# Optimization experiments

Measured on AMD Instinct MI355X. Metric: run time of the kernel, lower is better.

The kernel has to match this reference:

```python
import jax, jax.numpy as jnp
import numpy as np

B_J0 = 0.01   # baseline threshold
DT = 1.0
BETA = 1.8    # adaptation strength
LENS = 0.5
SCALE = 6.0
HIGHT = 0.15
GAMMA = 0.5


def _gauss(x, mu, sigma):
    return jnp.exp(-(x - mu) ** 2 / (2.0 * sigma ** 2)) / jnp.sqrt(2.0 * jnp.pi) / sigma


@jax.custom_vjp
def spike_fn(x):
    return (x > 0).astype(x.dtype)


def _spike_fwd(x):
    return spike_fn(x), x


def _spike_bwd(x, g):
    # multi-gaussian surrogate gradient (config.gradient_type == 'MG')
    temp = (_gauss(x, 0.0, LENS) * (1.0 + HIGHT)
            - _gauss(x, LENS, SCALE * LENS) * HIGHT
            - _gauss(x, -LENS, SCALE * LENS) * HIGHT)
    return (g * temp * GAMMA,)


spike_fn.defvjp(_spike_fwd, _spike_bwd)


def setup_inputs() -> dict:
    key = jax.random.key(0)
    ks = jax.random.split(key, 20)
    Bt, T, I, H, O = 256, 250, 700, 128, 20
    f32 = jnp.float32
    return {
        'x': jax.random.uniform(ks[0], (Bt, T, I), dtype=f32),
        'mask': jnp.ones((2, H, H), dtype=f32),
        'w_ih1': (jax.random.normal(ks[1], (I, H), dtype=f32) / np.sqrt(I).astype(np.float32)),
        'b_ih1': jnp.zeros((H,), f32),
        'w_h1h1': (jax.random.normal(ks[2], (H, H), dtype=f32) / np.sqrt(H).astype(np.float32)),
        'b_h1h1': jnp.zeros((H,), f32),
        'w_h1h2': (jax.random.normal(ks[3], (H, H), dtype=f32) / np.sqrt(H).astype(np.float32)),
        'b_h1h2': jnp.zeros((H,), f32),
        'w_h2h2': (jax.random.normal(ks[4], (H, H), dtype=f32) / np.sqrt(H).astype(np.float32)),
        'b_h2h2': jnp.zeros((H,), f32),
        'w_h2o': (jax.random.normal(ks[5], (H, O), dtype=f32) / np.sqrt(H).astype(np.float32)),
        'b_h2o': jnp.zeros((O,), f32),
        'tau_adp_h1': 150.0 + 10.0 * jax.random.normal(ks[6], (H,), dtype=f32),
        'tau_adp_h2': 150.0 + 10.0 * jax.random.normal(ks[7], (H,), dtype=f32),
        'tau_m_h1': 20.0 + 5.0 * jax.random.normal(ks[8], (H,), dtype=f32),
        'tau_m_h2': 20.0 + 5.0 * jax.random.normal(ks[9], (H,), dtype=f32),
        'tau_m_o': 20.0 + 5.0 * jax.random.normal(ks[10], (O,), dtype=f32),
        'hid1_mem0': jax.random.uniform(ks[11], (Bt, H), dtype=f32),
        'hid2_mem0': jax.random.uniform(ks[12], (Bt, H), dtype=f32),
        'out_mem0': jax.random.uniform(ks[13], (Bt, O), dtype=f32),
    }


def _forward(x, mask, w_ih1, b_ih1, w_h1h1, b_h1h1, w_h1h2, b_h1h2,
             w_h2h2, b_h2h2, w_h2o, b_h2o, tau_adp_h1, tau_adp_h2,
             tau_m_h1, tau_m_h2, tau_m_o, hid1_mem0, hid2_mem0, out_mem0):
    Bt, T, _ = x.shape
    H = w_ih1.shape[1]
    O = w_h2o.shape[1]
    # dropout mask applied to recurrent weights (weights stored [in, out])
    w11 = w_h1h1 * mask[0]
    w22 = w_h2h2 * mask[1]
    a1 = jnp.exp(-DT / tau_m_h1)
    r1 = jnp.exp(-DT / tau_adp_h1)
    a2 = jnp.exp(-DT / tau_m_h2)
    r2 = jnp.exp(-DT / tau_adp_h2)
    ao = jnp.exp(-DT / tau_m_o)
    # precompute input projection for all timesteps: [T, B, H]
    xin = jnp.einsum('bti,ih->tbh', x, w_ih1) + b_ih1

    def step(carry, inps):
        h1m, h1s, h2m, h2s, om, b1, b2, acc, s1, s2 = carry
        xt, t = inps
        # layer 1 (adaptive LIF)
        i1 = xt + h1s @ w11 + b_h1h1
        b1 = r1 * b1 + (1.0 - r1) * h1s
        B1 = B_J0 + BETA * b1
        h1m = h1m * a1 + (1.0 - a1) * i1 - B1 * h1s * DT
        h1s = spike_fn(h1m - B1)
        s1 = s1 + h1s
        # layer 2 (adaptive LIF)
        i2 = h1s @ w_h1h2 + b_h1h2 + h2s @ w22 + b_h2h2
        b2 = r2 * b2 + (1.0 - r2) * h2s
        B2 = B_J0 + BETA * b2
        h2m = h2m * a2 + (1.0 - a2) * i2 - B2 * h2s * DT
        h2s = spike_fn(h2m - B2)
        s2 = s2 + h2s
        # leaky-integrator readout (no spike)
        io = h2s @ w_h2o + b_h2o
        om = om * ao + (1.0 - ao) * io
        acc = acc + jnp.where(t > 10, jax.nn.softmax(om, axis=-1), 0.0)
        return (h1m, h1s, h2m, h2s, om, b1, b2, acc, s1, s2), None

    zH = jnp.zeros((Bt, H), x.dtype)
    carry0 = (hid1_mem0, zH, hid2_mem0, zH, out_mem0,
              jnp.full((Bt, H), B_J0, x.dtype), jnp.full((Bt, H), B_J0, x.dtype),
              jnp.zeros((Bt, O), x.dtype), zH, zH)
    carry, _ = jax.lax.scan(step, carry0, (xin, jnp.arange(T)))
    output, s1, s2 = carry[7], carry[8], carry[9]
    A_norm = jnp.sum(jnp.abs(w11)) + jnp.sum(jnp.abs(w22))
    return output, s1 / T, s2 / T, A_norm


def reference(x, mask, w_ih1, b_ih1, w_h1h1, b_h1h1, w_h1h2, b_h1h2,
              w_h2h2, b_h2h2, w_h2o, b_h2o, tau_adp_h1, tau_adp_h2,
              tau_m_h1, tau_m_h2, tau_m_o, hid1_mem0, hid2_mem0, out_mem0):
    return _forward(x, mask, w_ih1, b_ih1, w_h1h1, b_h1h1, w_h1h2, b_h1h2,
                    w_h2h2, b_h2h2, w_h2o, b_h2o, tau_adp_h1, tau_adp_h2,
                    tau_m_h1, tau_m_h2, tau_m_o, hid1_mem0, hid2_mem0, out_mem0)
```

## Files before the change

### kernel.cpp

```cpp
#include <hip/hip_runtime.h>
#include <math.h>

#define TT 250
#define BT 256
#define HN 128
#define ON 20
#define KIN 700
#define NKT 22

#define XIN_OFF 0
#define WPKH_OFF 8192000
#define WPKL_OFF 8237056

typedef __attribute__((ext_vector_type(8))) short bf16x8;
typedef __attribute__((ext_vector_type(4))) float f32x4;

__device__ __forceinline__ unsigned short bf16rne(float f) {
    unsigned u = __float_as_uint(f);
    unsigned r = u + 0x7fffu + ((u >> 16) & 1u);
    return (unsigned short)(r >> 16);
}
__device__ __forceinline__ void hilo(float v, short& h, short& l) {
    unsigned short hh = bf16rne(v);
    float vh = __uint_as_float((unsigned)hh << 16);
    h = (short)hh;
    l = (short)bf16rne(v - vh);
}

__global__ __launch_bounds__(256) void packw(const float* __restrict__ w,
                                             unsigned short* __restrict__ ph,
                                             unsigned short* __restrict__ pl) {
    int i = blockIdx.x * 256 + threadIdx.x;
    int k = i >> 7, c = i & 127;
    float v = (k < KIN) ? w[k * HN + c] : 0.f;
    short h, l;
    hilo(v, h, l);
    int dst = (((k >> 5) * 8 + (c >> 4)) * 64 + (((k >> 3) & 3) * 16 + (c & 15))) * 8 + (k & 7);
    ph[dst] = (unsigned short)h;
    pl[dst] = (unsigned short)l;
}

__global__ __launch_bounds__(256) void gemm_in(const float* __restrict__ x,
        const bf16x8* __restrict__ wph, const bf16x8* __restrict__ wpl,
        const float* __restrict__ bias1, const float* __restrict__ bias2,
        float* __restrict__ xin) {
    const int tid = threadIdx.x;
    const int w = tid >> 6, lane = tid & 63;
    const int q = lane >> 4, li = lane & 15;
    const long mrow = (long)blockIdx.x * 64 + w * 16 + li;
    const float* xr = x + mrow * KIN + q * 8;

    float b12[8];
#pragma unroll
    for (int nt = 0; nt < 8; nt++) {
        int col = nt * 16 + li;
        b12[nt] = bias1[col] + bias2[col];
    }

    f32x4 acc[8];
#pragma unroll
    for (int nt = 0; nt < 8; nt++) acc[nt] = (f32x4){0.f, 0.f, 0.f, 0.f};

    for (int kt = 0; kt < NKT; kt++) {
        float av[8];
        const float* p = xr + kt * 32;
        *(float4*)&av[0] = *(const float4*)p;
        if (kt == NKT - 1 && q == 3) {
            av[4] = 0.f; av[5] = 0.f; av[6] = 0.f; av[7] = 0.f;
        } else {
            *(float4*)&av[4] = *(const float4*)(p + 4);
        }
        bf16x8 ah, al;
#pragma unroll
        for (int j = 0; j < 8; j++) {
            short h, l;
            hilo(av[j], h, l);
            ah[j] = h; al[j] = l;
        }
#pragma unroll
        for (int nt = 0; nt < 8; nt++) {
            bf16x8 bh = wph[(kt * 8 + nt) * 64 + lane];
            bf16x8 bl = wpl[(kt * 8 + nt) * 64 + lane];
            acc[nt] = __builtin_amdgcn_mfma_f32_16x16x32_bf16(ah, bh, acc[nt], 0, 0, 0);
            acc[nt] = __builtin_amdgcn_mfma_f32_16x16x32_bf16(al, bh, acc[nt], 0, 0, 0);
            acc[nt] = __builtin_amdgcn_mfma_f32_16x16x32_bf16(ah, bl, acc[nt], 0, 0, 0);
        }
    }

#pragma unroll
    for (int r = 0; r < 4; r++) {
        int m = blockIdx.x * 64 + w * 16 + q * 4 + r;
        int bq = (int)(((unsigned long long)m * 67109ull) >> 24);
        int tt = m - bq * 250;
        float* dst = xin + ((size_t)tt * BT + bq) * HN;
#pragma unroll
        for (int nt = 0; nt < 8; nt++) dst[nt * 16 + li] = acc[nt][r] + b12[nt];
    }
}

__global__ __launch_bounds__(512, 2) void snn_scan(
    const float* __restrict__ xin, const float* __restrict__ mask,
    const float* __restrict__ w_h1h1, const float* __restrict__ w_h1h2,
    const float* __restrict__ b_h1h2, const float* __restrict__ w_h2h2,
    const float* __restrict__ b_h2h2, const float* __restrict__ w_h2o,
    const float* __restrict__ b_h2o, const float* __restrict__ tau_adp1,
    const float* __restrict__ tau_adp2, const float* __restrict__ taum1,
    const float* __restrict__ taum2, const float* __restrict__ taumo,
    const float* __restrict__ h1m0, const float* __restrict__ h2m0,
    const float* __restrict__ om0, float* __restrict__ out) {

    __shared__ __align__(16) unsigned short sA1[2 * 2048];
    __shared__ __align__(16) unsigned short sA2[2048];
    __shared__ float omb[16 * ON];
    __shared__ float red[8];

    const int tid = threadIdx.x;
    const int w = tid >> 6, lane = tid & 63;
    const int q = lane >> 4, li = lane & 15;
    const int col = w * 16 + li;
    const int r0 = blockIdx.x * 16;

    bf16x8 h11[4], l11[4], h22[4], l22[4], h12[4], l12[4], hO[4], lO[4];
    const int ocol = (w == 6) ? li : 16 + li;
    const bool oval = (w >= 6) && (ocol < ON);
    float pn = 0.f;
#pragma unroll
    for (int kt = 0; kt < 4; kt++) {
#pragma unroll
        for (int j = 0; j < 8; j++) {
            const int k = kt * 32 + q * 8 + j;
            const int idx = k * HN + col;
            float v11 = w_h1h1[idx] * mask[idx];
            float v22 = w_h2h2[idx] * mask[HN * HN + idx];
            float v12 = w_h1h2[idx];
            pn += fabsf(v11) + fabsf(v22);
            short hh, ll;
            hilo(v11, hh, ll); h11[kt][j] = hh; l11[kt][j] = ll;
            hilo(v22, hh, ll); h22[kt][j] = hh; l22[kt][j] = ll;
            hilo(v12, hh, ll); h12[kt][j] = hh; l12[kt][j] = ll;
            float vO = oval ? w_h2o[k * ON + ocol] : 0.f;
            hilo(vO, hh, ll); hO[kt][j] = hh; lO[kt][j] = ll;
        }
    }

    const float a1 = expf(-1.f / taum1[col]);
    const float r1 = expf(-1.f / tau_adp1[col]);
    const float a2 = expf(-1.f / taum2[col]);
    const float r2 = expf(-1.f / tau_adp2[col]);
    const float cc2 = b_h1h2[col] + b_h2h2[col];
    float h1m[4], h2m[4], b1[4], b2[4], c1[4], c2n[4];
    unsigned s1bits = 0, s2bits = 0;
#pragma unroll
    for (int r = 0; r < 4; r++) {
        h1m[r] = h1m0[(r0 + q * 4 + r) * HN + col];
        h2m[r] = h2m0[(r0 + q * 4 + r) * HN + col];
        b1[r] = 0.01f; b2[r] = 0.01f; c1[r] = 0.f; c2n[r] = 0.f;
    }
    const float ao = oval ? expf(-1.f / taumo[ocol]) : 0.f;
    const float bo = oval ? b_h2o[ocol] : 0.f;
    float om[4];
#pragma unroll
    for (int r = 0; r < 4; r++)
        om[r] = oval ? om0[(r0 + q * 4 + r) * ON + ocol] : 0.f;
    const int sm = lane >> 2, ob = (lane & 3) * 5;
    float accs[5] = {0.f, 0.f, 0.f, 0.f, 0.f};

    {
        unsigned* z1 = (unsigned*)sA1;
        unsigned* z2 = (unsigned*)sA2;
        z1[tid] = 0u; z1[tid + 512] = 0u;
        z2[tid] = 0u; z2[tid + 512] = 0u;
    }

#pragma unroll
    for (int off = 32; off > 0; off >>= 1) pn += __shfl_down(pn, off);
    if (lane == 0) red[w] = pn;
    __syncthreads();
    if (tid == 0 && blockIdx.x == 0) {
        float s = 0.f;
#pragma unroll
        for (int i = 0; i < 8; i++) s += red[i];
        out[70656] = s;
    }

    const int wbase = (w >> 1) * 512 + (((2 * w + (li >> 3)) & 3) * 16 + q * 4) * 8 + (li & 7);

    const bf16x8* sa1v = (const bf16x8*)sA1;
    const bf16x8* sa2v = (const bf16x8*)sA2;
    const unsigned short ONE = 0x3F80u;

    for (int t = 0; t < TT; t++) {
        const int rb = (t & 1) * 256;
        const int wb = ((t + 1) & 1) * 2048;

        float xt[4];
#pragma unroll
        for (int r = 0; r < 4; r++)
            xt[r] = xin[((size_t)t * BT + r0 + q * 4 + r) * HN + col];

        bf16x8 f1[4], f2[4];
#pragma unroll
        for (int kt = 0; kt < 4; kt++) {
            f1[kt] = sa1v[rb + kt * 64 + lane];
            f2[kt] = sa2v[kt * 64 + lane];
        }
        f32x4 aI = {0.f, 0.f, 0.f, 0.f}, aG = {0.f, 0.f, 0.f, 0.f};
#pragma unroll
        for (int kt = 0; kt < 4; kt++) {
            aI = __builtin_amdgcn_mfma_f32_16x16x32_bf16(f1[kt], h11[kt], aI, 0, 0, 0);
            aI = __builtin_amdgcn_mfma_f32_16x16x32_bf16(f1[kt], l11[kt], aI, 0, 0, 0);
            aG = __builtin_amdgcn_mfma_f32_16x16x32_bf16(f2[kt], h22[kt], aG, 0, 0, 0);
            aG = __builtin_amdgcn_mfma_f32_16x16x32_bf16(f2[kt], l22[kt], aG, 0, 0, 0);
        }
        if (w >= 6) {
            f32x4 aO = {0.f, 0.f, 0.f, 0.f};
#pragma unroll
            for (int kt = 0; kt < 4; kt++) {
                aO = __builtin_amdgcn_mfma_f32_16x16x32_bf16(f2[kt], hO[kt], aO, 0, 0, 0);
                aO = __builtin_amdgcn_mfma_f32_16x16x32_bf16(f2[kt], lO[kt], aO, 0, 0, 0);
            }
            if (t >= 1) {
#pragma unroll
                for (int r = 0; r < 4; r++) {
                    om[r] = ao * om[r] + (1.f - ao) * (bo + aO[r]);
                    if (oval) omb[(q * 4 + r) * ON + ocol] = om[r];
                }
            }
        }
#pragma unroll
        for (int r = 0; r < 4; r++) {
            const float sv = (float)((s1bits >> r) & 1u);
            const float i1 = xt[r] + aI[r];
            b1[r] = r1 * b1[r] + (1.f - r1) * sv;
            const float B = 0.01f + 1.8f * b1[r];
            h1m[r] = a1 * h1m[r] + (1.f - a1) * i1 - B * sv;
            const bool sp = (h1m[r] - B) > 0.f;
            s1bits = sp ? (s1bits | (1u << r)) : (s1bits & ~(1u << r));
            c1[r] += sp ? 1.f : 0.f;
            sA1[wb + wbase + r * 8] = sp ? ONE : (unsigned short)0;
        }
        __syncthreads();

        bf16x8 g1[4];
#pragma unroll
        for (int kt = 0; kt < 4; kt++) g1[kt] = sa1v[(wb >> 3) + kt * 64 + lane];
        f32x4 aJ = {0.f, 0.f, 0.f, 0.f};
#pragma unroll
        for (int kt = 0; kt < 4; kt++) {
            aJ = __builtin_amdgcn_mfma_f32_16x16x32_bf16(g1[kt], h12[kt], aJ, 0, 0, 0);
            aJ = __builtin_amdgcn_mfma_f32_16x16x32_bf16(g1[kt], l12[kt], aJ, 0, 0, 0);
        }
        if (w == 7 && t >= 12) {
            float v[5], e[5];
            float mx = -1e30f;
#pragma unroll
            for (int i = 0; i < 5; i++) { v[i] = omb[sm * ON + ob + i]; mx = fmaxf(mx, v[i]); }
            mx = fmaxf(mx, __shfl_xor(mx, 1));
            mx = fmaxf(mx, __shfl_xor(mx, 2));
            float se = 0.f;
#pragma unroll
            for (int i = 0; i < 5; i++) { e[i] = __expf(v[i] - mx); se += e[i]; }
            se += __shfl_xor(se, 1);
            se += __shfl_xor(se, 2);
            const float inv = 1.f / se;
#pragma unroll
            for (int i = 0; i < 5; i++) accs[i] += e[i] * inv;
        }
#pragma unroll
        for (int r = 0; r < 4; r++) {
            const float sv = (float)((s2bits >> r) & 1u);
            const float i2 = aJ[r] + aG[r] + cc2;
            b2[r] = r2 * b2[r] + (1.f - r2) * sv;
            const float B = 0.01f + 1.8f * b2[r];
            h2m[r] = a2 * h2m[r] + (1.f - a2) * i2 - B * sv;
            const bool sp = (h2m[r] - B) > 0.f;
            s2bits = sp ? (s2bits | (1u << r)) : (s2bits & ~(1u << r));
            c2n[r] += sp ? 1.f : 0.f;
            sA2[wbase + r * 8] = sp ? ONE : (unsigned short)0;
        }
        __syncthreads();
    }

    if (w >= 6) {
        bf16x8 f2[4];
#pragma unroll
        for (int kt = 0; kt < 4; kt++) f2[kt] = sa2v[kt * 64 + lane];
        f32x4 aO = {0.f, 0.f, 0.f, 0.f};
#pragma unroll
        for (int kt = 0; kt < 4; kt++) {
            aO = __builtin_amdgcn_mfma_f32_16x16x32_bf16(f2[kt], hO[kt], aO, 0, 0, 0);
            aO = __builtin_amdgcn_mfma_f32_16x16x32_bf16(f2[kt], lO[kt], aO, 0, 0, 0);
        }
#pragma unroll
        for (int r = 0; r < 4; r++) {
            om[r] = ao * om[r] + (1.f - ao) * (bo + aO[r]);
            if (oval) omb[(q * 4 + r) * ON + ocol] = om[r];
        }
    }
    __syncthreads();
    if (w == 7) {
        float v[5], e[5];
        float mx = -1e30f;
#pragma unroll
        for (int i = 0; i < 5; i++) { v[i] = omb[sm * ON + ob + i]; mx = fmaxf(mx, v[i]); }
        mx = fmaxf(mx, __shfl_xor(mx, 1));
        mx = fmaxf(mx, __shfl_xor(mx, 2));
        float se = 0.f;
#pragma unroll
        for (int i = 0; i < 5; i++) { e[i] = __expf(v[i] - mx); se += e[i]; }
        se += __shfl_xor(se, 1);
        se += __shfl_xor(se, 2);
        const float inv = 1.f / se;
#pragma unroll
        for (int i = 0; i < 5; i++) out[(r0 + sm) * ON + ob + i] = accs[i] + e[i] * inv;
    }
#pragma unroll
    for (int r = 0; r < 4; r++) {
        out[5120 + (r0 + q * 4 + r) * HN + col] = c1[r] * (1.f / 250.f);
        out[37888 + (r0 + q * 4 + r) * HN + col] = c2n[r] * (1.f / 250.f);
    }
}

extern "C" void kernel_launch(void* const* d_in, const int* in_sizes, int n_in,
                              void* d_out, int out_size, void* d_ws, size_t ws_size,
                              hipStream_t stream) {
    const float* x        = (const float*)d_in[0];
    const float* mask     = (const float*)d_in[1];
    const float* w_ih1    = (const float*)d_in[2];
    const float* b_ih1    = (const float*)d_in[3];
    const float* w_h1h1   = (const float*)d_in[4];
    const float* b_h1h1   = (const float*)d_in[5];
    const float* w_h1h2   = (const float*)d_in[6];
    const float* b_h1h2   = (const float*)d_in[7];
    const float* w_h2h2   = (const float*)d_in[8];
    const float* b_h2h2   = (const float*)d_in[9];
    const float* w_h2o    = (const float*)d_in[10];
    const float* b_h2o    = (const float*)d_in[11];
    const float* tau_adp1 = (const float*)d_in[12];
    const float* tau_adp2 = (const float*)d_in[13];
    const float* taum1    = (const float*)d_in[14];
    const float* taum2    = (const float*)d_in[15];
    const float* taumo    = (const float*)d_in[16];
    const float* h1m0     = (const float*)d_in[17];
    const float* h2m0     = (const float*)d_in[18];
    const float* om0      = (const float*)d_in[19];
    float* out = (float*)d_out;
    float* ws  = (float*)d_ws;

    float* xin = ws + XIN_OFF;
    unsigned short* wph = (unsigned short*)(ws + WPKH_OFF);
    unsigned short* wpl = (unsigned short*)(ws + WPKL_OFF);

    packw<<<352, 256, 0, stream>>>(w_ih1, wph, wpl);
    gemm_in<<<1000, 256, 0, stream>>>(x, (const bf16x8*)wph, (const bf16x8*)wpl,
                                      b_ih1, b_h1h1, xin);
    snn_scan<<<16, 512, 0, stream>>>(xin, mask, w_h1h1, w_h1h2, b_h1h2, w_h2h2,
                                     b_h2h2, w_h2o, b_h2o, tau_adp1, tau_adp2,
                                     taum1, taum2, taumo, h1m0, h2m0, om0, out);
}
```

Before: 655.8 us.

## Split scan hi/lo MFMA across 16 waves and stage GEMM weights in LDS

The recurrent scan kernel doubles its block to 1024 threads. Eight waves compute the high-bf16 weight products and run the neuron updates, while eight more waves compute the low-bf16 products and exchange partial sums through shared memory. Layer-2 work is skewed one step behind layer 1, so each timestep needs two barriers instead of a double-buffered spike array, and the readout softmax moves to a dedicated wave. The input GEMM now double-buffers the packed weight tiles in LDS instead of reading them from global memory per wave. The trade-offs are extra shared-memory traffic, larger blocks and more complex pipelining that could introduce off-by-one timing errors.

```diff
diff --git a/kernel.cpp b/kernel.cpp
--- a/kernel.cpp
+++ b/kernel.cpp
@@ -44,6 +44,7 @@
         const bf16x8* __restrict__ wph, const bf16x8* __restrict__ wpl,
         const float* __restrict__ bias1, const float* __restrict__ bias2,
         float* __restrict__ xin) {
+    __shared__ __align__(16) short Bs[2][2][4096];
     const int tid = threadIdx.x;
     const int w = tid >> 6, lane = tid & 63;
     const int q = lane >> 4, li = lane & 15;
@@ -52,39 +53,54 @@
 
     float b12[8];
 #pragma unroll
-    for (int nt = 0; nt < 8; nt++) {
-        int col = nt * 16 + li;
-        b12[nt] = bias1[col] + bias2[col];
-    }
+    for (int nt = 0; nt < 8; nt++) b12[nt] = bias1[nt * 16 + li] + bias2[nt * 16 + li];
 
     f32x4 acc[8];
 #pragma unroll
     for (int nt = 0; nt < 8; nt++) acc[nt] = (f32x4){0.f, 0.f, 0.f, 0.f};
 
+    {
+        bf16x8* dh = (bf16x8*)Bs[0][0];
+        bf16x8* dl = (bf16x8*)Bs[0][1];
+        dh[tid] = wph[tid]; dh[tid + 256] = wph[tid + 256];
+        dl[tid] = wpl[tid]; dl[tid + 256] = wpl[tid + 256];
+    }
+    __syncthreads();
+
     for (int kt = 0; kt < NKT; kt++) {
+        const int cur = kt & 1;
+        const bool more = (kt + 1 < NKT);
+        bf16x8 nh0, nh1, nl0, nl1;
+        if (more) {
+            const int base = (kt + 1) * 512 + tid;
+            nh0 = wph[base]; nh1 = wph[base + 256];
+            nl0 = wpl[base]; nl1 = wpl[base + 256];
+        }
         float av[8];
-        const float* p = xr + kt * 32;
-        *(float4*)&av[0] = *(const float4*)p;
-        if (kt == NKT - 1 && q == 3) {
-            av[4] = 0.f; av[5] = 0.f; av[6] = 0.f; av[7] = 0.f;
-        } else {
-            *(float4*)&av[4] = *(const float4*)(p + 4);
-        }
+        *(float4*)&av[0] = *(const float4*)(xr + kt * 32);
+        if (kt == NKT - 1 && q == 3) { av[4] = 0.f; av[5] = 0.f; av[6] = 0.f; av[7] = 0.f; }
+        else *(float4*)&av[4] = *(const float4*)(xr + kt * 32 + 4);
         bf16x8 ah, al;
 #pragma unroll
-        for (int j = 0; j < 8; j++) {
-            short h, l;
-            hilo(av[j], h, l);
-            ah[j] = h; al[j] = l;
-        }
+        for (int j = 0; j < 8; j++) { short h, l; hilo(av[j], h, l); ah[j] = h; al[j] = l; }
+
+        const bf16x8* bh = (const bf16x8*)Bs[cur][0];
+        const bf16x8* bl = (const bf16x8*)Bs[cur][1];
 #pragma unroll
         for (int nt = 0; nt < 8; nt++) {
-            bf16x8 bh = wph[(kt * 8 + nt) * 64 + lane];
-            bf16x8 bl = wpl[(kt * 8 + nt) * 64 + lane];
-            acc[nt] = __builtin_amdgcn_mfma_f32_16x16x32_bf16(ah, bh, acc[nt], 0, 0, 0);
-            acc[nt] = __builtin_amdgcn_mfma_f32_16x16x32_bf16(al, bh, acc[nt], 0, 0, 0);
-            acc[nt] = __builtin_amdgcn_mfma_f32_16x16x32_bf16(ah, bl, acc[nt], 0, 0, 0);
-        }
+            bf16x8 vh = bh[nt * 64 + lane];
+            bf16x8 vl = bl[nt * 64 + lane];
+            acc[nt] = __builtin_amdgcn_mfma_f32_16x16x32_bf16(ah, vh, acc[nt], 0, 0, 0);
+            acc[nt] = __builtin_amdgcn_mfma_f32_16x16x32_bf16(al, vh, acc[nt], 0, 0, 0);
+            acc[nt] = __builtin_amdgcn_mfma_f32_16x16x32_bf16(ah, vl, acc[nt], 0, 0, 0);
+        }
+        if (more) {
+            bf16x8* dh = (bf16x8*)Bs[cur ^ 1][0];
+            bf16x8* dl = (bf16x8*)Bs[cur ^ 1][1];
+            dh[tid] = nh0; dh[tid + 256] = nh1;
+            dl[tid] = nl0; dl[tid + 256] = nl1;
+        }
+        __syncthreads();
     }
 
 #pragma unroll
@@ -98,7 +114,9 @@
     }
 }
 
-__global__ __launch_bounds__(512, 2) void snn_scan(
+#define PST 20
+
+__global__ __launch_bounds__(1024) void snn_scan(
     const float* __restrict__ xin, const float* __restrict__ mask,
     const float* __restrict__ w_h1h1, const float* __restrict__ w_h1h2,
     const float* __restrict__ b_h1h2, const float* __restrict__ w_h2h2,
@@ -109,20 +127,28 @@
     const float* __restrict__ h1m0, const float* __restrict__ h2m0,
     const float* __restrict__ om0, float* __restrict__ out) {
 
-    __shared__ __align__(16) unsigned short sA1[2 * 2048];
-    __shared__ __align__(16) unsigned short sA2[2048];
-    __shared__ float omb[16 * ON];
-    __shared__ float red[8];
+    __shared__ __align__(16) unsigned short sF1[2048];
+    __shared__ __align__(16) unsigned short sF2[2048];
+    __shared__ __align__(16) float P11[HN * PST];
+    __shared__ __align__(16) float P12[HN * PST];
+    __shared__ __align__(16) float P22[HN * PST];
+    __shared__ __align__(16) float Ohi[ON * PST];
+    __shared__ __align__(16) float Olo[ON * PST];
+    __shared__ float red[16];
 
     const int tid = threadIdx.x;
     const int w = tid >> 6, lane = tid & 63;
     const int q = lane >> 4, li = lane & 15;
-    const int col = w * 16 + li;
+    const bool ishi = (w < 8);
+    const int g = w & 7;
+    const int col = g * 16 + li;
     const int r0 = blockIdx.x * 16;
 
-    bf16x8 h11[4], l11[4], h22[4], l22[4], h12[4], l12[4], hO[4], lO[4];
-    const int ocol = (w == 6) ? li : 16 + li;
-    const bool oval = (w >= 6) && (ocol < ON);
+    bf16x8 f11[4], f12[4], f22[4], fO[4];
+    const bool whoW = (w >= 12);
+    const int ocol = (w < 14) ? li : 16 + li;
+    const bool oval = whoW && (ocol < ON);
+    const bool oHi = (w == 12) || (w == 14);
     float pn = 0.f;
 #pragma unroll
     for (int kt = 0; kt < 4; kt++) {
@@ -133,44 +159,49 @@
             float v11 = w_h1h1[idx] * mask[idx];
             float v22 = w_h2h2[idx] * mask[HN * HN + idx];
             float v12 = w_h1h2[idx];
-            pn += fabsf(v11) + fabsf(v22);
-            short hh, ll;
-            hilo(v11, hh, ll); h11[kt][j] = hh; l11[kt][j] = ll;
-            hilo(v22, hh, ll); h22[kt][j] = hh; l22[kt][j] = ll;
-            hilo(v12, hh, ll); h12[kt][j] = hh; l12[kt][j] = ll;
+            if (ishi) pn += fabsf(v11) + fabsf(v22);
+            short h, l;
+            hilo(v11, h, l); f11[kt][j] = ishi ? h : l;
+            hilo(v22, h, l); f22[kt][j] = ishi ? h : l;
+            hilo(v12, h, l); f12[kt][j] = ishi ? h : l;
             float vO = oval ? w_h2o[k * ON + ocol] : 0.f;
-            hilo(vO, hh, ll); hO[kt][j] = hh; lO[kt][j] = ll;
-        }
-    }
-
-    const float a1 = expf(-1.f / taum1[col]);
-    const float r1 = expf(-1.f / tau_adp1[col]);
-    const float a2 = expf(-1.f / taum2[col]);
-    const float r2 = expf(-1.f / tau_adp2[col]);
-    const float cc2 = b_h1h2[col] + b_h2h2[col];
-    float h1m[4], h2m[4], b1[4], b2[4], c1[4], c2n[4];
+            hilo(vO, h, l); fO[kt][j] = oHi ? h : l;
+        }
+    }
+
+    float a1 = 0.f, r1c = 0.f, a2 = 0.f, r2c = 0.f, cc2 = 0.f;
+    float h1m[4], h2m[4], b1a[4], b2a[4], c1[4], c2n[4], xt[4];
     unsigned s1bits = 0, s2bits = 0;
-#pragma unroll
-    for (int r = 0; r < 4; r++) {
-        h1m[r] = h1m0[(r0 + q * 4 + r) * HN + col];
-        h2m[r] = h2m0[(r0 + q * 4 + r) * HN + col];
-        b1[r] = 0.01f; b2[r] = 0.01f; c1[r] = 0.f; c2n[r] = 0.f;
-    }
-    const float ao = oval ? expf(-1.f / taumo[ocol]) : 0.f;
-    const float bo = oval ? b_h2o[ocol] : 0.f;
-    float om[4];
-#pragma unroll
-    for (int r = 0; r < 4; r++)
-        om[r] = oval ? om0[(r0 + q * 4 + r) * ON + ocol] : 0.f;
+    if (ishi) {
+        a1 = expf(-1.f / taum1[col]);
+        r1c = expf(-1.f / tau_adp1[col]);
+        a2 = expf(-1.f / taum2[col]);
+        r2c = expf(-1.f / tau_adp2[col]);
+        cc2 = b_h1h2[col] + b_h2h2[col];
+#pragma unroll
+        for (int r = 0; r < 4; r++) {
+            h1m[r] = h1m0[(r0 + q * 4 + r) * HN + col];
+            h2m[r] = h2m0[(r0 + q * 4 + r) * HN + col];
+            b1a[r] = 0.01f; b2a[r] = 0.01f; c1[r] = 0.f; c2n[r] = 0.f;
+            xt[r] = xin[(size_t)(r0 + q * 4 + r) * HN + col];
+        }
+    }
     const int sm = lane >> 2, ob = (lane & 3) * 5;
-    float accs[5] = {0.f, 0.f, 0.f, 0.f, 0.f};
-
-    {
-        unsigned* z1 = (unsigned*)sA1;
-        unsigned* z2 = (unsigned*)sA2;
-        z1[tid] = 0u; z1[tid + 512] = 0u;
-        z2[tid] = 0u; z2[tid + 512] = 0u;
-    }
+    float om[5], accs[5], aoc[5], bjoc[5];
+    if (w == 15) {
+#pragma unroll
+        for (int i = 0; i < 5; i++) {
+            aoc[i] = expf(-1.f / taumo[ob + i]);
+            bjoc[i] = b_h2o[ob + i];
+            om[i] = om0[(r0 + sm) * ON + ob + i];
+            accs[i] = 0.f;
+        }
+    }
+
+    ((unsigned*)sF1)[tid] = 0u;
+    ((unsigned*)sF2)[tid] = 0u;
+    for (int i = tid; i < HN * PST; i += 1024) { P11[i] = 0.f; P12[i] = 0.f; P22[i] = 0.f; }
+    for (int i = tid; i < ON * PST; i += 1024) { Ohi[i] = 0.f; Olo[i] = 0.f; }
 
 #pragma unroll
     for (int off = 32; off > 0; off >>= 1) pn += __shfl_down(pn, off);
@@ -183,141 +214,194 @@
         out[70656] = s;
     }
 
-    const int wbase = (w >> 1) * 512 + (((2 * w + (li >> 3)) & 3) * 16 + q * 4) * 8 + (li & 7);
-
-    const bf16x8* sa1v = (const bf16x8*)sA1;
-    const bf16x8* sa2v = (const bf16x8*)sA2;
+    const int wbase = (w >> 1) * 512 + ((((2 * w + (li >> 3)) & 3) * 16 + q * 4) * 8) + (li & 7);
+    const int pidx = col * PST + q * 4;
+    const bf16x8* s1v = (const bf16x8*)sF1;
+    const bf16x8* s2v = (const bf16x8*)sF2;
     const unsigned short ONE = 0x3F80u;
 
+    f32x4 aI = {0.f, 0.f, 0.f, 0.f}, aJ = {0.f, 0.f, 0.f, 0.f}, aG = {0.f, 0.f, 0.f, 0.f};
+
     for (int t = 0; t < TT; t++) {
-        const int rb = (t & 1) * 256;
-        const int wb = ((t + 1) & 1) * 2048;
-
-        float xt[4];
-#pragma unroll
-        for (int r = 0; r < 4; r++)
-            xt[r] = xin[((size_t)t * BT + r0 + q * 4 + r) * HN + col];
-
-        bf16x8 f1[4], f2[4];
-#pragma unroll
-        for (int kt = 0; kt < 4; kt++) {
-            f1[kt] = sa1v[rb + kt * 64 + lane];
-            f2[kt] = sa2v[kt * 64 + lane];
-        }
-        f32x4 aI = {0.f, 0.f, 0.f, 0.f}, aG = {0.f, 0.f, 0.f, 0.f};
-#pragma unroll
-        for (int kt = 0; kt < 4; kt++) {
-            aI = __builtin_amdgcn_mfma_f32_16x16x32_bf16(f1[kt], h11[kt], aI, 0, 0, 0);
-            aI = __builtin_amdgcn_mfma_f32_16x16x32_bf16(f1[kt], l11[kt], aI, 0, 0, 0);
-            aG = __builtin_amdgcn_mfma_f32_16x16x32_bf16(f2[kt], h22[kt], aG, 0, 0, 0);
-            aG = __builtin_amdgcn_mfma_f32_16x16x32_bf16(f2[kt], l22[kt], aG, 0, 0, 0);
-        }
-        if (w >= 6) {
-            f32x4 aO = {0.f, 0.f, 0.f, 0.f};
+        if (ishi) {
+            if (t >= 1) {
+                float4 pj = *(float4*)&P12[pidx];
+                float4 pg = *(float4*)&P22[pidx];
+#pragma unroll
+                for (int r = 0; r < 4; r++) {
+                    const float sv = (float)((s2bits >> r) & 1u);
+                    const float i2 = aJ[r] + pj[r] + aG[r] + pg[r] + cc2;
+                    b2a[r] = r2c * b2a[r] + (1.f - r2c) * sv;
+                    const float B = 0.01f + 1.8f * b2a[r];
+                    h2m[r] = a2 * h2m[r] + (1.f - a2) * i2 - B * sv;
+                    const bool sp = (h2m[r] - B) > 0.f;
+                    s2bits = sp ? (s2bits | (1u << r)) : (s2bits & ~(1u << r));
+                    c2n[r] += sp ? 1.f : 0.f;
+                    sF2[wbase + r * 8] = sp ? ONE : (unsigned short)0;
+                }
+            }
+            {
+                float4 pi = *(float4*)&P11[pidx];
+#pragma unroll
+                for (int r = 0; r < 4; r++) {
+                    const float sv = (float)((s1bits >> r) & 1u);
+                    const float i1 = xt[r] + aI[r] + pi[r];
+                    b1a[r] = r1c * b1a[r] + (1.f - r1c) * sv;
+                    const float B = 0.01f + 1.8f * b1a[r];
+                    h1m[r] = a1 * h1m[r] + (1.f - a1) * i1 - B * sv;
+                    const bool sp = (h1m[r] - B) > 0.f;
+                    s1bits = sp ? (s1bits | (1u << r)) : (s1bits & ~(1u << r));
+                    c1[r] += sp ? 1.f : 0.f;
+                    sF1[wbase + r * 8] = sp ? ONE : (unsigned short)0;
+                }
+            }
+        } else if (w == 15 && t >= 2) {
+            float e[5];
+#pragma unroll
+            for (int i = 0; i < 5; i++) {
+                const float io = bjoc[i] + Ohi[(ob + i) * PST + sm] + Olo[(ob + i) * PST + sm];
+                om[i] = aoc[i] * om[i] + (1.f - aoc[i]) * io;
+            }
+            if (t >= 13) {
+                float mx = om[0];
+#pragma unroll
+                for (int i = 1; i < 5; i++) mx = fmaxf(mx, om[i]);
+                mx = fmaxf(mx, __shfl_xor(mx, 1));
+                mx = fmaxf(mx, __shfl_xor(mx, 2));
+                float se = 0.f;
+#pragma unroll
+                for (int i = 0; i < 5; i++) { e[i] = __expf(om[i] - mx); se += e[i]; }
+                se += __shfl_xor(se, 1);
+                se += __shfl_xor(se, 2);
+                const float inv = 1.f / se;
+#pragma unroll
+                for (int i = 0; i < 5; i++) accs[i] += e[i] * inv;
+            }
+        }
+        __syncthreads();
+
+        if (ishi) {
+            const int tn = (t < TT - 1) ? t + 1 : t;
+#pragma unroll
+            for (int r = 0; r < 4; r++)
+                xt[r] = xin[((size_t)tn * BT + r0 + q * 4 + r) * HN + col];
+            aI = (f32x4){0.f, 0.f, 0.f, 0.f};
+            aJ = (f32x4){0.f, 0.f, 0.f, 0.f};
+            aG = (f32x4){0.f, 0.f, 0.f, 0.f};
 #pragma unroll
             for (int kt = 0; kt < 4; kt++) {
-                aO = __builtin_amdgcn_mfma_f32_16x16x32_bf16(f2[kt], hO[kt], aO, 0, 0, 0);
-                aO = __builtin_amdgcn_mfma_f32_16x16x32_bf16(f2[kt], lO[kt], aO, 0, 0, 0);
-            }
-            if (t >= 1) {
-#pragma unroll
-                for (int r = 0; r < 4; r++) {
-                    om[r] = ao * om[r] + (1.f - ao) * (bo + aO[r]);
-                    if (oval) omb[(q * 4 + r) * ON + ocol] = om[r];
+                bf16x8 s1f = s1v[kt * 64 + lane];
+                bf16x8 s2f = s2v[kt * 64 + lane];
+                aI = __builtin_amdgcn_mfma_f32_16x16x32_bf16(s1f, f11[kt], aI, 0, 0, 0);
+                aJ = __builtin_amdgcn_mfma_f32_16x16x32_bf16(s1f, f12[kt], aJ, 0, 0, 0);
+                aG = __builtin_amdgcn_mfma_f32_16x16x32_bf16(s2f, f22[kt], aG, 0, 0, 0);
+            }
+        } else {
+            f32x4 pI = {0.f, 0.f, 0.f, 0.f}, pJ = {0.f, 0.f, 0.f, 0.f}, pG = {0.f, 0.f, 0.f, 0.f};
+#pragma unroll
+            for (int kt = 0; kt < 4; kt++) {
+                bf16x8 s1f = s1v[kt * 64 + lane];
+                bf16x8 s2f = s2v[kt * 64 + lane];
+                pI = __builtin_amdgcn_mfma_f32_16x16x32_bf16(s1f, f11[kt], pI, 0, 0, 0);
+                pJ = __builtin_amdgcn_mfma_f32_16x16x32_bf16(s1f, f12[kt], pJ, 0, 0, 0);
+                pG = __builtin_amdgcn_mfma_f32_16x16x32_bf16(s2f, f22[kt], pG, 0, 0, 0);
+            }
+            *(float4*)&P11[pidx] = *(float4*)&pI;
+            *(float4*)&P12[pidx] = *(float4*)&pJ;
+            *(float4*)&P22[pidx] = *(float4*)&pG;
+            if (whoW) {
+                f32x4 pO = {0.f, 0.f, 0.f, 0.f};
+#pragma unroll
+                for (int kt = 0; kt < 4; kt++) {
+                    bf16x8 s2f = s2v[kt * 64 + lane];
+                    pO = __builtin_amdgcn_mfma_f32_16x16x32_bf16(s2f, fO[kt], pO, 0, 0, 0);
                 }
-            }
-        }
-#pragma unroll
-        for (int r = 0; r < 4; r++) {
-            const float sv = (float)((s1bits >> r) & 1u);
-            const float i1 = xt[r] + aI[r];
-            b1[r] = r1 * b1[r] + (1.f - r1) * sv;
-            const float B = 0.01f + 1.8f * b1[r];
-            h1m[r] = a1 * h1m[r] + (1.f - a1) * i1 - B * sv;
-            const bool sp = (h1m[r] - B) > 0.f;
-            s1bits = sp ? (s1bits | (1u << r)) : (s1bits & ~(1u << r));
-            c1[r] += sp ? 1.f : 0.f;
-            sA1[wb + wbase + r * 8] = sp ? ONE : (unsigned short)0;
+                if (oval) {
+                    float* O = oHi ? Ohi : Olo;
+                    *(float4*)&O[ocol * PST + q * 4] = *(float4*)&pO;
+                }
+            }
         }
         __syncthreads();
-
-        bf16x8 g1[4];
-#pragma unroll
-        for (int kt = 0; kt < 4; kt++) g1[kt] = sa1v[(wb >> 3) + kt * 64 + lane];
-        f32x4 aJ = {0.f, 0.f, 0.f, 0.f};
-#pragma unroll
-        for (int kt = 0; kt < 4; kt++) {
-            aJ = __builtin_amdgcn_mfma_f32_16x16x32_bf16(g1[kt], h12[kt], aJ, 0, 0, 0);
-            aJ = __builtin_amdgcn_mfma_f32_16x16x32_bf16(g1[kt], l12[kt], aJ, 0, 0, 0);
-        }
-        if (w == 7 && t >= 12) {
-            float v[5], e[5];
-            float mx = -1e30f;
-#pragma unroll
-            for (int i = 0; i < 5; i++) { v[i] = omb[sm * ON + ob + i]; mx = fmaxf(mx, v[i]); }
-            mx = fmaxf(mx, __shfl_xor(mx, 1));
-            mx = fmaxf(mx, __shfl_xor(mx, 2));
-            float se = 0.f;
-#pragma unroll
-            for (int i = 0; i < 5; i++) { e[i] = __expf(v[i] - mx); se += e[i]; }
-            se += __shfl_xor(se, 1);
-            se += __shfl_xor(se, 2);
-            const float inv = 1.f / se;
-#pragma unroll
-            for (int i = 0; i < 5; i++) accs[i] += e[i] * inv;
-        }
+    }
+
+    if (ishi) {
+        float4 pj = *(float4*)&P12[pidx];
+        float4 pg = *(float4*)&P22[pidx];
 #pragma unroll
         for (int r = 0; r < 4; r++) {
             const float sv = (float)((s2bits >> r) & 1u);
-            const float i2 = aJ[r] + aG[r] + cc2;
-            b2[r] = r2 * b2[r] + (1.f - r2) * sv;
-            const float B = 0.01f + 1.8f * b2[r];
+            const float i2 = aJ[r] + pj[r] + aG[r] + pg[r] + cc2;
+            b2a[r] = r2c * b2a[r] + (1.f - r2c) * sv;
+            const float B = 0.01f + 1.8f * b2a[r];
             h2m[r] = a2 * h2m[r] + (1.f - a2) * i2 - B * sv;
             const bool sp = (h2m[r] - B) > 0.f;
-            s2bits = sp ? (s2bits | (1u << r)) : (s2bits & ~(1u << r));
             c2n[r] += sp ? 1.f : 0.f;
-            sA2[wbase + r * 8] = sp ? ONE : (unsigned short)0;
-        }
-        __syncthreads();
-    }
-
-    if (w >= 6) {
-        bf16x8 f2[4];
-#pragma unroll
-        for (int kt = 0; kt < 4; kt++) f2[kt] = sa2v[kt * 64 + lane];
-        f32x4 aO = {0.f, 0.f, 0.f, 0.f};
-#pragma unroll
-        for (int kt = 0; kt < 4; kt++) {
-            aO = __builtin_amdgcn_mfma_f32_16x16x32_bf16(f2[kt], hO[kt], aO, 0, 0, 0);
-            aO = __builtin_amdgcn_mfma_f32_16x16x32_bf16(f2[kt], lO[kt], aO, 0, 0, 0);
-        }
-#pragma unroll
-        for (int r = 0; r < 4; r++) {
-            om[r] = ao * om[r] + (1.f - ao) * (bo + aO[r]);
-            if (oval) omb[(q * 4 + r) * ON + ocol] = om[r];
-        }
-    }
-    __syncthreads();
-    if (w == 7) {
-        float v[5], e[5];
-        float mx = -1e30f;
-#pragma unroll
-        for (int i = 0; i < 5; i++) { v[i] = omb[sm * ON + ob + i]; mx = fmaxf(mx, v[i]); }
+            sF2[wbase + r * 8] = sp ? ONE : (unsigned short)0;
+        }
+    } else if (w == 15) {
+        float e[5];
+#pragma unroll
+        for (int i = 0; i < 5; i++) {
+            const float io = bjoc[i] + Ohi[(ob + i) * PST + sm] + Olo[(ob + i) * PST + sm];
+            om[i] = aoc[i] * om[i] + (1.f - aoc[i]) * io;
+        }
+        float mx = om[0];
+#pragma unroll
+        for (int i = 1; i < 5; i++) mx = fmaxf(mx, om[i]);
         mx = fmaxf(mx, __shfl_xor(mx, 1));
         mx = fmaxf(mx, __shfl_xor(mx, 2));
         float se = 0.f;
 #pragma unroll
-        for (int i = 0; i < 5; i++) { e[i] = __expf(v[i] - mx); se += e[i]; }
+        for (int i = 0; i < 5; i++) { e[i] = __expf(om[i] - mx); se += e[i]; }
         se += __shfl_xor(se, 1);
         se += __shfl_xor(se, 2);
         const float inv = 1.f / se;
 #pragma unroll
-        for (int i = 0; i < 5; i++) out[(r0 + sm) * ON + ob + i] = accs[i] + e[i] * inv;
-    }
-#pragma unroll
-    for (int r = 0; r < 4; r++) {
-        out[5120 + (r0 + q * 4 + r) * HN + col] = c1[r] * (1.f / 250.f);
-        out[37888 + (r0 + q * 4 + r) * HN + col] = c2n[r] * (1.f / 250.f);
+        for (int i = 0; i < 5; i++) accs[i] += e[i] * inv;
+    }
+    __syncthreads();
+    if (whoW) {
+        f32x4 pO = {0.f, 0.f, 0.f, 0.f};
+#pragma unroll
+        for (int kt = 0; kt < 4; kt++) {
+            bf16x8 s2f = s2v[kt * 64 + lane];
+            pO = __builtin_amdgcn_mfma_f32_16x16x32_bf16(s2f, fO[kt], pO, 0, 0, 0);
+        }
+        if (oval) {
+            float* O = oHi ? Ohi : Olo;
+            *(float4*)&O[ocol * PST + q * 4] = *(float4*)&pO;
+        }
+    }
+    __syncthreads();
+    if (w == 15) {
+        float e[5];
+#pragma unroll
+        for (int i = 0; i < 5; i++) {
+            const float io = bjoc[i] + Ohi[(ob + i) * PST + sm] + Olo[(ob + i) * PST + sm];
+            om[i] = aoc[i] * om[i] + (1.f - aoc[i]) * io;
+        }
+        float mx = om[0];
+#pragma unroll
+        for (int i = 1; i < 5; i++) mx = fmaxf(mx, om[i]);
+        mx = fmaxf(mx, __shfl_xor(mx, 1));
+        mx = fmaxf(mx, __shfl_xor(mx, 2));
+        float se = 0.f;
+#pragma unroll
+        for (int i = 0; i < 5; i++) { e[i] = __expf(om[i] - mx); se += e[i]; }
+        se += __shfl_xor(se, 1);
+        se += __shfl_xor(se, 2);
+        const float inv = 1.f / se;
+#pragma unroll
+        for (int i = 0; i < 5; i++)
+            out[(r0 + sm) * ON + ob + i] = accs[i] + e[i] * inv;
+    }
+    if (ishi) {
+#pragma unroll
+        for (int r = 0; r < 4; r++) {
+            out[5120 + (r0 + q * 4 + r) * HN + col] = c1[r] * (1.f / 250.f);
+            out[37888 + (r0 + q * 4 + r) * HN + col] = c2n[r] * (1.f / 250.f);
+        }
     }
 }
 
@@ -354,7 +438,7 @@
     packw<<<352, 256, 0, stream>>>(w_ih1, wph, wpl);
     gemm_in<<<1000, 256, 0, stream>>>(x, (const bf16x8*)wph, (const bf16x8*)wpl,
                                       b_ih1, b_h1h1, xin);
-    snn_scan<<<16, 512, 0, stream>>>(xin, mask, w_h1h1, w_h1h2, b_h1h2, w_h2h2,
-                                     b_h2h2, w_h2o, b_h2o, tau_adp1, tau_adp2,
-                                     taum1, taum2, taumo, h1m0, h2m0, om0, out);
-}
+    snn_scan<<<16, 1024, 0, stream>>>(xin, mask, w_h1h1, w_h1h2, b_h1h2, w_h2h2,
+                                      b_h2h2, w_h2o, b_h2o, tau_adp1, tau_adp2,
+                                      taum1, taum2, taumo, h1m0, h2m0, om0, out);
+}
```

After: 1.432 ms. 2.18x slower.
